# Kernel optimization log

Measured on AMD Instinct MI355X. Metric: run time of the kernel, lower is better.

The kernel has to match this reference:

```python
import jax, jax.numpy as jnp
import numpy as np

N_SEQ = 512      # n: number of generation steps (rows of x_tensor)
N_POOL = 4096    # candidate node pool size (rows of f_tensor / a_tensor)
N_FEAT = 20
E = 64           # n_node_embed
G = 128          # n_graph_embed
S = 16           # n_seq_embed
ALPHA = 20       # n_seq_alphabets


def setup_inputs() -> dict:
    key = jax.random.key(0)
    ks = jax.random.split(key, 16)
    f32 = jnp.float32

    def lin(k, fan_in, shape):
        return jax.random.normal(k, shape, f32) / jnp.sqrt(jnp.asarray(fan_in, f32))

    return {
        "x_tensor": jax.random.normal(ks[0], (N_SEQ, ALPHA), f32),
        "f_tensor": jax.random.normal(ks[1], (N_POOL, N_FEAT), f32),
        "a_tensor": jax.random.uniform(ks[2], (N_POOL, N_POOL), f32),
        "d_tensor": jax.random.uniform(ks[3], (N_POOL, N_POOL), f32),
        "w_feat": lin(ks[4], N_FEAT, (N_FEAT, E)),
        "b_feat": lin(ks[5], N_FEAT, (E,)),
        "w_gcn1": lin(ks[6], E, (E, E)),   # GCN W1, bias=False
        "w_gcn2": lin(ks[7], E, (E, E)),   # GCN W1, bias=False
        "w_graph": lin(ks[8], E, (E, G)),
        "b_graph": lin(ks[9], E, (G,)),
        "w_gate": lin(ks[10], E, (E, G)),
        "b_gate": lin(ks[11], E, (G,)),
        "w_edge": lin(ks[12], 2 * E + S + G, (2 * E + S + G, 1)),
        "b_edge": lin(ks[13], 2 * E + S + G, (1,)),
        "w_seq": lin(ks[14], ALPHA, (ALPHA, S)),
        "b_seq": lin(ks[15], ALPHA, (S,)),
    }


def reference(x_tensor, f_tensor, a_tensor, d_tensor,
              w_feat, b_feat, w_gcn1, w_gcn2,
              w_graph, b_graph, w_gate, b_gate,
              w_edge, b_edge, w_seq, b_seq):
    n = x_tensor.shape[0]
    Np = f_tensor.shape[0]
    e = w_feat.shape[1]
    g_dim = w_graph.shape[1]

    seq_embed = x_tensor @ w_seq + b_seq                 # [n, S]
    f_nodes_in = f_tensor @ w_feat + b_feat              # [Np, E]
    dAd = (d_tensor @ a_tensor) @ d_tensor               # gcn1: D A D
    h_nodes_in = (dAd @ jax.nn.relu(f_nodes_in)) @ w_gcn1  # [Np, E]

    # Chain graph at step k has k+1 nodes; A = I + sub/super diagonals.
    # Degrees: 1 (k==0), 2 at endpoints, 3 interior. Dh[k, i] = deg^{-1/2}, masked.
    ii = jnp.arange(n)
    kk = ii[:, None]
    jj = ii[None, :]
    deg = jnp.where((jj == 0) | (jj == kk), 2.0, 3.0)
    deg = jnp.where(kk == 0, 1.0, deg)
    Dh = jnp.where(jj <= kk, deg ** -0.5, 0.0).astype(x_tensor.dtype)  # [n, n]

    def step(carry, k):
        mask, idxs, h_last, h_graph = carry
        z = jnp.concatenate([
            h_nodes_in,
            jnp.broadcast_to(h_last, (Np, e)),
            jnp.broadcast_to(seq_embed[k], (Np, seq_embed.shape[1])),
            jnp.broadcast_to(h_graph, (Np, g_dim)),
        ], axis=1)                                        # [Np, 2E+S+G]
        score = ((jax.nn.relu(z) * mask[:, None]) @ w_edge)[:, 0] + b_edge[0]
        idx = jnp.argmax(score)
        mask = mask.at[idx].set(0.0)
        idxs = idxs.at[k].set(idx.astype(jnp.int32))

        # gcn2 on the chain graph over the k+1 selected nodes (band-structured).
        F_sel = f_nodes_in[idxs]                          # [n, E]; rows > k masked by dh
        dh = Dh[k]                                        # [n]
        gmat = dh[:, None] * F_sel
        g_up = jnp.pad(gmat, ((0, 1), (0, 0)))[1:]        # g[i+1]
        g_dn = jnp.pad(gmat, ((1, 0), (0, 0)))[:-1]       # g[i-1]
        dF = dh[:, None] * (gmat + g_up + g_dn)           # (D A D) F on the chain
        h_nodes = dF @ w_gcn2                             # [n, E]; rows > k are zero
        h_last_new = jnp.take(h_nodes, k, axis=0)

        valid = (jnp.arange(n) <= k).astype(h_nodes.dtype)[:, None]
        hg = h_nodes @ w_graph + b_graph
        gg = h_nodes @ w_gate + b_gate
        h_graph_new = jnp.sum(hg * jax.nn.sigmoid(gg) * valid, axis=0)
        return (mask, idxs, h_last_new, h_graph_new), score

    init = (jnp.ones(Np, x_tensor.dtype),
            jnp.zeros(n, jnp.int32),
            jnp.zeros(e, x_tensor.dtype),
            jnp.zeros(g_dim, x_tensor.dtype))
    (_, idxs, _, _), scores = jax.lax.scan(step, init, jnp.arange(n))
    return scores, idxs
```

## Files before the change

kernel.cpp:

```cpp
#include <hip/hip_runtime.h>
#include <math.h>

#define NPOOL 4096
#define NSEQ  512
#define NF    20
#define EDIM  64
#define GDIM  128
#define SDIM  16
#define ALPH  20
#define SPLITK 16
#define KSLICE (NPOOL / SPLITK)

__device__ __forceinline__ double relu_d(double x){ return x > 0.0 ? x : 0.0; }
__device__ __forceinline__ double sigm_d(double x){ return 1.0 / (1.0 + exp(-x)); }

__global__ __launch_bounds__(256) void k_prep(const float* __restrict__ f, const float* __restrict__ wf,
                       const float* __restrict__ bf, double* __restrict__ Fin, double* __restrict__ R,
                       double* __restrict__ T1z) {
    int t = blockIdx.x * 256 + threadIdx.x;
    int i = t >> 6, e = t & 63;
    double acc = (double)bf[e];
#pragma unroll
    for (int j = 0; j < NF; ++j)
        acc += (double)f[i * NF + j] * (double)wf[j * EDIM + e];
    Fin[t] = acc;
    R[t] = acc > 0.0 ? acc : 0.0;
    T1z[t] = 0.0;
}

__global__ __launch_bounds__(256) void k_seqe(const float* __restrict__ x, const float* __restrict__ wsq,
                       const float* __restrict__ bsq, double* __restrict__ seqe, int* __restrict__ rank) {
    int t = blockIdx.x * 256 + threadIdx.x;
    int k = t >> 4, s = t & 15;
    double acc = (double)bsq[s];
#pragma unroll
    for (int q = 0; q < ALPH; ++q)
        acc += (double)x[k * ALPH + q] * (double)wsq[q * SDIM + s];
    seqe[t] = acc;
    if (t < NPOOL) rank[t] = 1 << 30;
}

__global__ __launch_bounds__(256) void k_zero(double* __restrict__ buf) {
    buf[(size_t)blockIdx.x * 256 + threadIdx.x] = 0.0;
}

__global__ __launch_bounds__(256, 4) void gemm_f64_v3(const float* __restrict__ A, const double* __restrict__ B,
                                                      double* __restrict__ C) {
    __shared__ double As[32][66];
    __shared__ double Bs[32][66];
    int t  = threadIdx.x;
    int tx = t & 15;
    int ty = t >> 4;
    int row0 = blockIdx.x * 64;
    int k0   = blockIdx.y * KSLICE;
    double acc[4][4] = {};
    for (int kt = k0; kt < k0 + KSLICE; kt += 32) {
        {
            int r = t >> 2, kq = t & 3;
            const float* Ap = A + (size_t)(row0 + r) * NPOOL + kt + kq * 8;
            float4 f0 = *(const float4*)Ap;
            float4 f1 = *(const float4*)(Ap + 4);
            int kb = kq * 8;
            As[kb + 0][r] = (double)f0.x; As[kb + 1][r] = (double)f0.y;
            As[kb + 2][r] = (double)f0.z; As[kb + 3][r] = (double)f0.w;
            As[kb + 4][r] = (double)f1.x; As[kb + 5][r] = (double)f1.y;
            As[kb + 6][r] = (double)f1.z; As[kb + 7][r] = (double)f1.w;
        }
#pragma unroll
        for (int it = 0; it < 8; ++it) {
            int l = t + 256 * it;
            int kr = l >> 6, cc = l & 63;
            Bs[kr][cc] = B[(size_t)(kt + kr) * 64 + cc];
        }
        __syncthreads();
#pragma unroll
        for (int kk = 0; kk < 32; ++kk) {
            double2 a01 = *(const double2*)&As[kk][2 * ty];
            double2 a23 = *(const double2*)&As[kk][2 * ty + 32];
            double2 b01 = *(const double2*)&Bs[kk][2 * tx];
            double2 b23 = *(const double2*)&Bs[kk][2 * tx + 32];
            double a[4] = {a01.x, a01.y, a23.x, a23.y};
            double b[4] = {b01.x, b01.y, b23.x, b23.y};
#pragma unroll
            for (int i = 0; i < 4; ++i)
#pragma unroll
                for (int j = 0; j < 4; ++j)
                    acc[i][j] = fma(a[i], b[j], acc[i][j]);
        }
        __syncthreads();
    }
    int rr[4] = {2 * ty, 2 * ty + 1, 2 * ty + 32, 2 * ty + 33};
    int cc[4] = {2 * tx, 2 * tx + 1, 2 * tx + 32, 2 * tx + 33};
#pragma unroll
    for (int i = 0; i < 4; ++i)
#pragma unroll
        for (int j = 0; j < 4; ++j)
            unsafeAtomicAdd(&C[(size_t)(row0 + rr[i]) * 64 + cc[j]], acc[i][j]);
}

__global__ __launch_bounds__(256) void k_head(const double* __restrict__ T3, const float* __restrict__ w1,
                       const float* __restrict__ we, double* __restrict__ s) {
    int row = (blockIdx.x * 256 + threadIdx.x) >> 6;
    int e = threadIdx.x & 63;
    const double* r = T3 + (size_t)row * 64;
    double h = 0.0;
#pragma unroll
    for (int c = 0; c < 64; ++c)
        h += r[c] * (double)w1[c * 64 + e];
    double p = (h > 0.0 ? h : 0.0) * (double)we[e];
    for (int off = 32; off; off >>= 1) p += __shfl_down(p, off, 64);
    if (e == 0) s[row] = p;
}

__global__ __launch_bounds__(1024) void k_sort2(const double* __restrict__ s, int* __restrict__ order,
                        double* __restrict__ skey, int* __restrict__ orderB) {
    __shared__ unsigned long long keys[NPOOL];
    __shared__ int idxs[NPOOL];
    __shared__ unsigned long long ck[1024];
    __shared__ int ci[1024];
    __shared__ unsigned int hist[256];
    __shared__ unsigned int cntHi, cntEq;
    __shared__ unsigned long long prefix_s;
    __shared__ int K_s, fb_s;
    int t = threadIdx.x;
    for (int i = t; i < NPOOL; i += 1024) {
        double v = s[i] + 0.0;
        unsigned long long b = (unsigned long long)__double_as_longlong(v);
        unsigned long long m = (b >> 63) ? ~0ULL : 0x8000000000000000ULL;
        keys[i] = b ^ m;
        idxs[i] = i;
    }
    if (t == 0) { prefix_s = 0ULL; K_s = NSEQ; fb_s = 0; cntHi = 0; cntEq = 0; }
    __syncthreads();
    for (int shift = 56; shift >= 0; shift -= 8) {
        if (t < 256) hist[t] = 0;
        __syncthreads();
        unsigned long long pre = prefix_s;
        unsigned long long hmask = (shift == 56) ? 0ULL : (~0ULL << (shift + 8));
        for (int i = t; i < NPOOL; i += 1024) {
            unsigned long long kv = keys[i];
            if ((kv & hmask) == pre)
                atomicAdd(&hist[(unsigned)(kv >> shift) & 255u], 1u);
        }
        __syncthreads();
        if (t == 0) {
            int K = K_s;
            int cum = 0, b = 255;
            for (; b >= 0; --b) { cum += (int)hist[b]; if (cum >= K) break; }
            if (b < 0) { fb_s = 1; b = 0; }
            K_s = K - (cum - (int)hist[b]);
            prefix_s |= ((unsigned long long)(unsigned)b << shift);
        }
        __syncthreads();
    }
    unsigned long long T = prefix_s;
    for (int i = t; i < NPOOL; i += 1024) {
        unsigned long long kv = keys[i];
        if (kv > T) {
            unsigned p = atomicAdd(&cntHi, 1u);
            if (p < 1024u) { ck[p] = kv; ci[p] = i; }
        }
    }
    __syncthreads();
    unsigned base = cntHi;
    for (int i = t; i < NPOOL; i += 1024) {
        if (keys[i] == T) {
            unsigned p = atomicAdd(&cntEq, 1u);
            if (base + p < 1024u) { ck[base + p] = T; ci[base + p] = i; }
        }
    }
    __syncthreads();
    if (t == 0) {
        unsigned tot = cntHi + cntEq;
        if (cntHi >= (unsigned)NSEQ || tot < (unsigned)NSEQ || tot > 1024u) fb_s = 1;
    }
    __syncthreads();
    if (fb_s == 0) {
        unsigned tot = cntHi + cntEq;
        for (int i = (int)tot + t; i < 1024; i += 1024) { ck[i] = 0ULL; ci[i] = 0x7fffffff; }
        __syncthreads();
        for (int k2 = 2; k2 <= 1024; k2 <<= 1) {
            for (int j = k2 >> 1; j > 0; j >>= 1) {
                int l = t ^ j;
                if (l > t) {
                    unsigned long long ka = ck[t], kb = ck[l];
                    int ia = ci[t], ib = ci[l];
                    bool aBefore = (ka > kb) || (ka == kb && ia < ib);
                    bool asc = ((t & k2) == 0);
                    if (asc ? !aBefore : aBefore) { ck[t] = kb; ck[l] = ka; ci[t] = ib; ci[l] = ia; }
                }
                __syncthreads();
            }
        }
        if (t < NSEQ) {
            int id = ci[t];
            order[t] = id; skey[t] = s[id]; orderB[t] = ci[0];
        }
    } else {
        for (int k2 = 2; k2 <= NPOOL; k2 <<= 1) {
            for (int j = k2 >> 1; j > 0; j >>= 1) {
                for (int tt = t; tt < NPOOL; tt += 1024) {
                    int l = tt ^ j;
                    if (l > tt) {
                        unsigned long long ka = keys[tt], kb = keys[l];
                        int ia = idxs[tt], ib = idxs[l];
                        bool aBefore = (ka > kb) || (ka == kb && ia < ib);
                        bool asc = ((tt & k2) == 0);
                        if (asc ? !aBefore : aBefore) { keys[tt] = kb; keys[l] = ka; idxs[tt] = ib; idxs[l] = ia; }
                    }
                }
                __syncthreads();
            }
        }
        for (int tt = t; tt < NSEQ; tt += 1024) {
            int id = idxs[tt];
            order[tt] = id; skey[tt] = s[id]; orderB[tt] = idxs[0];
        }
    }
}

__global__ __launch_bounds__(256) void k_perk2(const double* __restrict__ Fin, const int* __restrict__ orderA,
                       const int* __restrict__ orderBv,
                       const float* __restrict__ w2, const float* __restrict__ wgr, const float* __restrict__ bgr,
                       const float* __restrict__ wga, const float* __restrict__ bga,
                       double* __restrict__ phi_inf, double* __restrict__ phi_pair, double* __restrict__ hlast) {
    const double r2 = 0.70710678118654752440;
    const double r3 = 0.57735026918962576451;
    __shared__ double u[4][64];
    __shared__ double comb[3][64];
    __shared__ double v[3][64];
    __shared__ double hgg[3][2][GDIM];
    int which = blockIdx.x >> 9;
    int k = blockIdx.x & (NSEQ - 1);
    const int* order = which ? orderBv : orderA;
    double* pi = phi_inf  + (size_t)which * NSEQ * GDIM;
    double* pp = phi_pair + (size_t)which * NSEQ * GDIM;
    double* hl = hlast    + (size_t)which * NSEQ * 64;
    int t = threadIdx.x;
    {
        int w = t >> 6, e = t & 63;
        int j = k - 3 + w;
        u[w][e] = (j >= 0) ? Fin[(size_t)order[j] * 64 + e] : 0.0;
    }
    __syncthreads();
    if (t < 192) {
        int w = t >> 6, e = t & 63;
        double dh_km3 = (k - 3 == 0) ? r2 : r3;
        double dh_km2 = (k - 2 == 0) ? r2 : r3;
        double dh_km1 = (k - 1 == 0) ? r2 : r3;
        double outer, c0, c1, c2, c3;
        if (w == 0) {
            outer = dh_km2; c0 = dh_km3; c1 = dh_km2; c2 = dh_km1; c3 = 0.0;
        } else if (w == 1) {
            outer = dh_km1; c0 = 0.0; c1 = dh_km2; c2 = dh_km1; c3 = r2;
        } else {
            if (k == 0) { outer = 1.0; c0 = c1 = c2 = 0.0; c3 = 1.0; }
            else        { outer = r2;  c0 = c1 = 0.0; c2 = dh_km1; c3 = r2; }
        }
        comb[w][e] = outer * (c0 * u[0][e] + c1 * u[1][e] + c2 * u[2][e] + c3 * u[3][e]);
    }
    __syncthreads();
    if (t < 192) {
        int w = t >> 6, e = t & 63;
        double acc = 0.0;
#pragma unroll
        for (int j = 0; j < 64; ++j)
            acc += comb[w][j] * (double)w2[j * 64 + e];
        v[w][e] = acc;
    }
    __syncthreads();
    for (int rep = 0; rep < 3; ++rep) {
        int d = t & 127, g = t >> 7;
        const float* W = g ? wga : wgr;
        const float* B = g ? bga : bgr;
        double acc = (double)B[d];
#pragma unroll
        for (int j = 0; j < 64; ++j)
            acc += v[rep][j] * (double)W[j * GDIM + d];
        hgg[rep][g][d] = acc;
    }
    __syncthreads();
    if (t < 128) {
        if (k >= 2) pi[(size_t)(k - 2) * GDIM + t] = hgg[0][0][t] * sigm_d(hgg[0][1][t]);
        double ppv = hgg[2][0][t] * sigm_d(hgg[2][1][t]);
        if (k >= 1) ppv += hgg[1][0][t] * sigm_d(hgg[1][1][t]);
        pp[(size_t)k * GDIM + t] = ppv;
    } else if (t < 192) {
        hl[(size_t)k * 64 + (t - 128)] = v[2][t - 128];
    }
}

__global__ __launch_bounds__(512) void k_scan2(const double* __restrict__ phi_inf, const double* __restrict__ phi_pair,
                       double* __restrict__ hgr) {
    __shared__ double sb[NSEQ];
    int which = blockIdx.x >> 7;
    int d = blockIdx.x & (GDIM - 1), t = threadIdx.x;
    const double* pi = phi_inf  + (size_t)which * NSEQ * GDIM;
    const double* pp = phi_pair + (size_t)which * NSEQ * GDIM;
    double* hg = hgr + (size_t)which * NSEQ * GDIM;
    sb[t] = (t >= 2) ? pi[(size_t)(t - 2) * GDIM + d] : 0.0;
    for (int off = 1; off < NSEQ; off <<= 1) {
        __syncthreads();
        double add = (t >= off) ? sb[t - off] : 0.0;
        __syncthreads();
        sb[t] += add;
    }
    __syncthreads();
    hg[(size_t)t * GDIM + d] = sb[t] + pp[(size_t)t * GDIM + d];
}

__global__ __launch_bounds__(64) void k_c2(const double* __restrict__ hlast, const double* __restrict__ hgr,
                   const double* __restrict__ seqe, const float* __restrict__ we,
                   double* __restrict__ cA, double* __restrict__ cB) {
    int which = blockIdx.x >> 9;
    int k = blockIdx.x & (NSEQ - 1), j = threadIdx.x;
    const double* hl = hlast + (size_t)which * NSEQ * 64;
    const double* hg = hgr   + (size_t)which * NSEQ * GDIM;
    double* c = which ? cB : cA;
    double ts = 0.0;
    if (k > 0) {
        ts += relu_d(hl[(size_t)(k - 1) * 64 + j]) * (double)we[64 + j];
        ts += relu_d(hg[(size_t)(k - 1) * GDIM + j]) * (double)we[144 + j];
        ts += relu_d(hg[(size_t)(k - 1) * GDIM + 64 + j]) * (double)we[208 + j];
    }
    if (j < 16) ts += relu_d(seqe[(size_t)k * SDIM + j]) * (double)we[128 + j];
    for (int off = 32; off; off >>= 1) ts += __shfl_down(ts, off, 64);
    if (j == 0) c[k] = ts;
}

__global__ __launch_bounds__(512) void k_verify2(const double* __restrict__ skey, const double* __restrict__ cA,
                         const double* __restrict__ cB, int* __restrict__ flagA, int* __restrict__ flagB) {
    __shared__ int bad;
    int t = threadIdx.x;
    if (t == 0) bad = 0;
    __syncthreads();
    if (blockIdx.x == 0) {
        if (t >= 1 && !(skey[t] + cA[t] > 0.0)) atomicOr(&bad, 1);
        __syncthreads();
        if (t == 0) flagA[0] = bad;
    } else {
        if (t >= 1 && (skey[1] + cB[t] > 0.0)) atomicOr(&bad, 1);
        __syncthreads();
        if (t == 0) flagB[0] = bad;
    }
}

__global__ __launch_bounds__(512) void k_select(const int* __restrict__ flagA, const int* __restrict__ flagB,
                        const double* __restrict__ cA, const double* __restrict__ cB,
                        const int* __restrict__ order, double* __restrict__ c,
                        int* __restrict__ idxs_sel, int* __restrict__ mode) {
    int t = threadIdx.x;
    if (flagA[0] == 0) {
        c[t] = cA[t]; idxs_sel[t] = order[t];
        if (t == 0) mode[0] = 0;
    } else if (flagB[0] == 0) {
        c[t] = cB[t]; idxs_sel[t] = order[0];
        if (t == 0) mode[0] = 1;
    } else {
        if (t == 0) mode[0] = 2;
    }
}

__global__ __launch_bounds__(256) void k_fallback(const int* __restrict__ mode,
        const double* __restrict__ Fin, const int* __restrict__ order, const double* __restrict__ skey,
        const double* __restrict__ seqe,
        const float* __restrict__ w2, const float* __restrict__ wgr, const float* __restrict__ bgr,
        const float* __restrict__ wga, const float* __restrict__ bga, const float* __restrict__ we,
        int* __restrict__ idxs_sel, double* __restrict__ c) {
    if (mode[0] != 2) return;
    const double r2 = 0.70710678118654752440;
    const double r3 = 0.57735026918962576451;
    __shared__ double u[4][64];
    __shared__ double comb[3][64];
    __shared__ double v[3][64];
    __shared__ double hgg[3][2][GDIM];
    __shared__ double Phi[GDIM], hgraph[GDIM], hlastS[64];
    __shared__ int selS, ptrS, minS_;
    int t = threadIdx.x;
    if (t < 64) { u[0][t] = u[1][t] = u[2][t] = u[3][t] = 0.0; hlastS[t] = 0.0; }
    if (t < 128) { Phi[t] = 0.0; hgraph[t] = 0.0; }
    if (t == 0) { ptrS = 0; minS_ = 0x7fffffff; }
    __syncthreads();
    for (int k = 0; k < NSEQ; ++k) {
        if (t < 64) {
            int j = t;
            double ts = relu_d(hlastS[j]) * (double)we[64 + j]
                      + relu_d(hgraph[j]) * (double)we[144 + j]
                      + relu_d(hgraph[64 + j]) * (double)we[208 + j];
            if (j < 16) ts += relu_d(seqe[(size_t)k * SDIM + j]) * (double)we[128 + j];
            for (int off = 32; off; off >>= 1) ts += __shfl_down(ts, off, 64);
            if (j == 0) {
                c[k] = ts;
                int ptr = ptrS, idx;
                if (ptr == 0) { idx = order[0]; minS_ = idx; ptrS = 1; }
                else if (skey[ptr] + ts > 0.0) {
                    idx = order[ptr];
                    if (idx < minS_) minS_ = idx;
                    ptrS = ptr + 1;
                } else idx = minS_;
                selS = idx;
                idxs_sel[k] = idx;
            }
        }
        __syncthreads();
        int idx = selS;
        if (t < 64) u[k & 3][t] = Fin[(size_t)idx * 64 + t];
        __syncthreads();
        if (t < 192) {
            int w = t >> 6, e = t & 63;
            double dh_km3 = (k - 3 == 0) ? r2 : r3;
            double dh_km2 = (k - 2 == 0) ? r2 : r3;
            double dh_km1 = (k - 1 == 0) ? r2 : r3;
            double outer, c0, c1, c2, c3;
            if (w == 0) {
                outer = dh_km2; c0 = dh_km3; c1 = dh_km2; c2 = dh_km1; c3 = 0.0;
            } else if (w == 1) {
                outer = dh_km1; c0 = 0.0; c1 = dh_km2; c2 = dh_km1; c3 = r2;
            } else {
                if (k == 0) { outer = 1.0; c0 = c1 = c2 = 0.0; c3 = 1.0; }
                else        { outer = r2;  c0 = c1 = 0.0; c2 = dh_km1; c3 = r2; }
            }
            double uu0 = u[(k - 3) & 3][e], uu1 = u[(k - 2) & 3][e], uu2 = u[(k - 1) & 3][e], uu3 = u[k & 3][e];
            comb[w][e] = outer * (c0 * uu0 + c1 * uu1 + c2 * uu2 + c3 * uu3);
        }
        __syncthreads();
        if (t < 192) {
            int w = t >> 6, e = t & 63;
            double acc = 0.0;
#pragma unroll
            for (int j = 0; j < 64; ++j)
                acc += comb[w][j] * (double)w2[j * 64 + e];
            v[w][e] = acc;
        }
        __syncthreads();
        for (int rep = 0; rep < 3; ++rep) {
            int d = t & 127, g = t >> 7;
            const float* W = g ? wga : wgr;
            const float* B = g ? bga : bgr;
            double acc = (double)B[d];
#pragma unroll
            for (int j = 0; j < 64; ++j)
                acc += v[rep][j] * (double)W[j * GDIM + d];
            hgg[rep][g][d] = acc;
        }
        __syncthreads();
        if (t < 128) {
            if (k >= 2) Phi[t] += hgg[0][0][t] * sigm_d(hgg[0][1][t]);
            double hg = Phi[t] + hgg[2][0][t] * sigm_d(hgg[2][1][t]);
            if (k >= 1) hg += hgg[1][0][t] * sigm_d(hgg[1][1][t]);
            hgraph[t] = hg;
        } else if (t < 192) {
            hlastS[t - 128] = v[2][t - 128];
        }
        __syncthreads();
    }
}

__global__ __launch_bounds__(256) void k_rank_set(const int* __restrict__ idxs_sel, int* __restrict__ rank,
                           float* __restrict__ out) {
    int t = blockIdx.x * 256 + threadIdx.x;
    if (t < NSEQ) {
        atomicMin(&rank[idxs_sel[t]], t);
        out[(size_t)NSEQ * NPOOL + t] = (float)idxs_sel[t];
    }
}

__global__ __launch_bounds__(256) void k_fill(const double* __restrict__ s, const double* __restrict__ c,
                       const int* __restrict__ rank, const float* __restrict__ be, float* __restrict__ out) {
    size_t t = (size_t)blockIdx.x * 256 + threadIdx.x;
    int k = (int)(t >> 12);
    int i = (int)(t & 4095);
    double bed = (double)be[0];
    bool masked = rank[i] < k;
    out[t] = masked ? (float)bed : (float)(s[i] + c[k] + bed);
}

extern "C" void kernel_launch(void* const* d_in, const int* in_sizes, int n_in,
                              void* d_out, int out_size, void* d_ws, size_t ws_size,
                              hipStream_t stream) {
    const float* x    = (const float*)d_in[0];
    const float* f    = (const float*)d_in[1];
    const float* amat = (const float*)d_in[2];
    const float* dmat = (const float*)d_in[3];
    const float* wf   = (const float*)d_in[4];
    const float* bf   = (const float*)d_in[5];
    const float* w1   = (const float*)d_in[6];
    const float* w2   = (const float*)d_in[7];
    const float* wgr  = (const float*)d_in[8];
    const float* bgr  = (const float*)d_in[9];
    const float* wga  = (const float*)d_in[10];
    const float* bga  = (const float*)d_in[11];
    const float* we   = (const float*)d_in[12];
    const float* be   = (const float*)d_in[13];
    const float* wsq  = (const float*)d_in[14];
    const float* bsq  = (const float*)d_in[15];
    float* out = (float*)d_out;

    char* p = (char*)d_ws;
    const size_t BIG = (size_t)NPOOL * 64 * sizeof(double);
    double* BUF0 = (double*)p; p += BIG;
    double* Fin  = (double*)p; p += BIG;
    double* BUF2 = (double*)p; p += BIG;
    double* seqe = (double*)p; p += (size_t)NSEQ * SDIM * sizeof(double);
    double* s    = (double*)p; p += (size_t)NPOOL * sizeof(double);
    double* skey = (double*)p; p += (size_t)NSEQ * sizeof(double);
    double* phi_inf  = (double*)p; p += 2 * (size_t)NSEQ * GDIM * sizeof(double);
    double* phi_pair = (double*)p; p += 2 * (size_t)NSEQ * GDIM * sizeof(double);
    double* hgr   = (double*)p; p += 2 * (size_t)NSEQ * GDIM * sizeof(double);
    double* hlast = (double*)p; p += 2 * (size_t)NSEQ * 64 * sizeof(double);
    double* cA    = (double*)p; p += (size_t)NSEQ * sizeof(double);
    double* cB    = (double*)p; p += (size_t)NSEQ * sizeof(double);
    double* c     = (double*)p; p += (size_t)NSEQ * sizeof(double);
    int* order    = (int*)p; p += 2048;
    int* orderB   = (int*)p; p += 2048;
    int* idxs_sel = (int*)p; p += 2048;
    int* rank     = (int*)p; p += (size_t)NPOOL * sizeof(int);
    int* flagA    = (int*)p; p += 256;
    int* flagB    = (int*)p; p += 256;
    int* mode     = (int*)p; p += 256;

    double* R  = BUF0;
    double* T1 = BUF2;
    double* T2 = BUF0;
    double* T3 = BUF2;

    dim3 ggrid(NPOOL / 64, SPLITK);

    k_prep<<<1024, 256, 0, stream>>>(f, wf, bf, Fin, R, T1);
    k_seqe<<<32, 256, 0, stream>>>(x, wsq, bsq, seqe, rank);

    gemm_f64_v3<<<ggrid, 256, 0, stream>>>(dmat, R, T1);
    k_zero<<<1024, 256, 0, stream>>>(T2);
    gemm_f64_v3<<<ggrid, 256, 0, stream>>>(amat, T1, T2);
    k_zero<<<1024, 256, 0, stream>>>(T3);
    gemm_f64_v3<<<ggrid, 256, 0, stream>>>(dmat, T2, T3);

    k_head<<<NPOOL / 4, 256, 0, stream>>>(T3, w1, we, s);
    k_sort2<<<1, 1024, 0, stream>>>(s, order, skey, orderB);

    k_perk2<<<2 * NSEQ, 256, 0, stream>>>(Fin, order, orderB, w2, wgr, bgr, wga, bga, phi_inf, phi_pair, hlast);
    k_scan2<<<2 * GDIM, 512, 0, stream>>>(phi_inf, phi_pair, hgr);
    k_c2<<<2 * NSEQ, 64, 0, stream>>>(hlast, hgr, seqe, we, cA, cB);
    k_verify2<<<2, 512, 0, stream>>>(skey, cA, cB, flagA, flagB);

    k_select<<<1, 512, 0, stream>>>(flagA, flagB, cA, cB, order, c, idxs_sel, mode);
    k_fallback<<<1, 256, 0, stream>>>(mode, Fin, order, skey, seqe, w2, wgr, bgr, wga, bga, we, idxs_sel, c);

    k_rank_set<<<2, 256, 0, stream>>>(idxs_sel, rank, out);
    k_fill<<<(NSEQ * NPOOL) / 256, 256, 0, stream>>>(s, c, rank, be, out);
}
```

Before: 525.7 us.

## Replace radix-select sort with register/shuffle bitonic sort on packed keys

The top-K selection kernel switches from a multi-pass radix histogram plus shared-memory bitonic sort to a full 4096-element bitonic sort. Each thread holds four packed keys (truncated score bits combined with the index) in registers, using wave shuffles for small strides and shared memory only for strides of 256 and above. A tie check falls back to the exact slow sort if truncation merges distinct scores. The head kernel also stages w1 in shared memory. This aims to cut the many barriers and atomics of the single-block sort, at the cost of more compare steps over all 4096 elements.

```diff
diff --git a/kernel.cpp b/kernel.cpp
--- a/kernel.cpp
+++ b/kernel.cpp
@@ -13,6 +13,12 @@
 
 __device__ __forceinline__ double relu_d(double x){ return x > 0.0 ? x : 0.0; }
 __device__ __forceinline__ double sigm_d(double x){ return 1.0 / (1.0 + exp(-x)); }
+
+__device__ __forceinline__ unsigned long long sortable_u64(double x) {
+    x = x + 0.0;
+    unsigned long long b = (unsigned long long)__double_as_longlong(x);
+    return b ^ ((b >> 63) ? ~0ULL : 0x8000000000000000ULL);
+}
 
 __global__ __launch_bounds__(256) void k_prep(const float* __restrict__ f, const float* __restrict__ wf,
                        const float* __restrict__ bf, double* __restrict__ Fin, double* __restrict__ R,
@@ -100,122 +106,139 @@
 
 __global__ __launch_bounds__(256) void k_head(const double* __restrict__ T3, const float* __restrict__ w1,
                        const float* __restrict__ we, double* __restrict__ s) {
-    int row = (blockIdx.x * 256 + threadIdx.x) >> 6;
-    int e = threadIdx.x & 63;
+    __shared__ float w1s[64 * 64];
+    int tt = threadIdx.x;
+    for (int i = tt; i < 64 * 64; i += 256) w1s[i] = w1[i];
+    __syncthreads();
+    int row = (blockIdx.x * 256 + tt) >> 6;
+    int e = tt & 63;
     const double* r = T3 + (size_t)row * 64;
     double h = 0.0;
 #pragma unroll
     for (int c = 0; c < 64; ++c)
-        h += r[c] * (double)w1[c * 64 + e];
+        h += r[c] * (double)w1s[c * 64 + e];
     double p = (h > 0.0 ? h : 0.0) * (double)we[e];
     for (int off = 32; off; off >>= 1) p += __shfl_down(p, off, 64);
     if (e == 0) s[row] = p;
 }
 
-__global__ __launch_bounds__(1024) void k_sort2(const double* __restrict__ s, int* __restrict__ order,
+__global__ __launch_bounds__(1024) void k_sort3(const double* __restrict__ s, int* __restrict__ order,
                         double* __restrict__ skey, int* __restrict__ orderB) {
-    __shared__ unsigned long long keys[NPOOL];
-    __shared__ int idxs[NPOOL];
-    __shared__ unsigned long long ck[1024];
-    __shared__ int ci[1024];
-    __shared__ unsigned int hist[256];
-    __shared__ unsigned int cntHi, cntEq;
-    __shared__ unsigned long long prefix_s;
-    __shared__ int K_s, fb_s;
+    __shared__ unsigned long long P[NPOOL];
+    __shared__ int idxF[NPOOL];
+    __shared__ int fbS;
     int t = threadIdx.x;
-    for (int i = t; i < NPOOL; i += 1024) {
-        double v = s[i] + 0.0;
-        unsigned long long b = (unsigned long long)__double_as_longlong(v);
-        unsigned long long m = (b >> 63) ? ~0ULL : 0x8000000000000000ULL;
-        keys[i] = b ^ m;
-        idxs[i] = i;
-    }
-    if (t == 0) { prefix_s = 0ULL; K_s = NSEQ; fb_s = 0; cntHi = 0; cntEq = 0; }
-    __syncthreads();
-    for (int shift = 56; shift >= 0; shift -= 8) {
-        if (t < 256) hist[t] = 0;
-        __syncthreads();
-        unsigned long long pre = prefix_s;
-        unsigned long long hmask = (shift == 56) ? 0ULL : (~0ULL << (shift + 8));
-        for (int i = t; i < NPOOL; i += 1024) {
-            unsigned long long kv = keys[i];
-            if ((kv & hmask) == pre)
-                atomicAdd(&hist[(unsigned)(kv >> shift) & 255u], 1u);
-        }
-        __syncthreads();
-        if (t == 0) {
-            int K = K_s;
-            int cum = 0, b = 255;
-            for (; b >= 0; --b) { cum += (int)hist[b]; if (cum >= K) break; }
-            if (b < 0) { fb_s = 1; b = 0; }
-            K_s = K - (cum - (int)hist[b]);
-            prefix_s |= ((unsigned long long)(unsigned)b << shift);
-        }
-        __syncthreads();
-    }
-    unsigned long long T = prefix_s;
-    for (int i = t; i < NPOOL; i += 1024) {
-        unsigned long long kv = keys[i];
-        if (kv > T) {
-            unsigned p = atomicAdd(&cntHi, 1u);
-            if (p < 1024u) { ck[p] = kv; ci[p] = i; }
-        }
-    }
-    __syncthreads();
-    unsigned base = cntHi;
-    for (int i = t; i < NPOOL; i += 1024) {
-        if (keys[i] == T) {
-            unsigned p = atomicAdd(&cntEq, 1u);
-            if (base + p < 1024u) { ck[base + p] = T; ci[base + p] = i; }
-        }
-    }
-    __syncthreads();
-    if (t == 0) {
-        unsigned tot = cntHi + cntEq;
-        if (cntHi >= (unsigned)NSEQ || tot < (unsigned)NSEQ || tot > 1024u) fb_s = 1;
-    }
-    __syncthreads();
-    if (fb_s == 0) {
-        unsigned tot = cntHi + cntEq;
-        for (int i = (int)tot + t; i < 1024; i += 1024) { ck[i] = 0ULL; ci[i] = 0x7fffffff; }
-        __syncthreads();
-        for (int k2 = 2; k2 <= 1024; k2 <<= 1) {
-            for (int j = k2 >> 1; j > 0; j >>= 1) {
-                int l = t ^ j;
-                if (l > t) {
-                    unsigned long long ka = ck[t], kb = ck[l];
-                    int ia = ci[t], ib = ci[l];
+    if (t == 0) fbS = 0;
+    unsigned long long v[4];
+#pragma unroll
+    for (int i = 0; i < 4; ++i) {
+        int e = 4 * t + i;
+        unsigned long long srt = sortable_u64(s[e]);
+        v[i] = ((~(srt >> 12)) << 12) | (unsigned long long)e;
+    }
+
+#define SHFL_ROUND(jj, kk)                                                        \
+    {                                                                             \
+        int lm = (int)((jj) >> 2);                                                \
+        _Pragma("unroll")                                                         \
+        for (int i = 0; i < 4; ++i) {                                             \
+            unsigned long long p = (unsigned long long)__shfl_xor((long long)v[i], lm, 64); \
+            unsigned e = 4u * (unsigned)t + (unsigned)i;                          \
+            bool takeMin = (((e & (jj)) == 0u) == ((e & (kk)) == 0u));            \
+            unsigned long long mn = v[i] < p ? v[i] : p;                          \
+            unsigned long long mx = v[i] < p ? p : v[i];                          \
+            v[i] = takeMin ? mn : mx;                                             \
+        }                                                                         \
+    }
+
+#define LOCAL_ROUNDS(kk)                                                          \
+    {                                                                             \
+        if ((kk) >= 4) {                                                          \
+            _Pragma("unroll")                                                     \
+            for (int i = 0; i < 2; ++i) {                                         \
+                unsigned e = 4u * (unsigned)t + (unsigned)i;                      \
+                bool asc = ((e & (kk)) == 0u);                                    \
+                unsigned long long a = v[i], b = v[i + 2];                        \
+                bool sw = asc ? (a > b) : (a < b);                                \
+                v[i] = sw ? b : a; v[i + 2] = sw ? a : b;                         \
+            }                                                                     \
+        }                                                                         \
+        _Pragma("unroll")                                                         \
+        for (int i = 0; i < 4; i += 2) {                                          \
+            unsigned e = 4u * (unsigned)t + (unsigned)i;                          \
+            bool asc = ((e & (kk)) == 0u);                                        \
+            unsigned long long a = v[i], b = v[i + 1];                            \
+            bool sw = asc ? (a > b) : (a < b);                                    \
+            v[i] = sw ? b : a; v[i + 1] = sw ? a : b;                             \
+        }                                                                         \
+    }
+
+    for (unsigned k = 2; k <= 256; k <<= 1) {
+        for (unsigned j = k >> 1; j >= 4; j >>= 1) SHFL_ROUND(j, k)
+        LOCAL_ROUNDS(k)
+    }
+    for (unsigned k = 512; k <= 4096; k <<= 1) {
+        for (unsigned j = k >> 1; j >= 256; j >>= 1) {
+            __syncthreads();
+            P[4 * t + 0] = v[0]; P[4 * t + 1] = v[1];
+            P[4 * t + 2] = v[2]; P[4 * t + 3] = v[3];
+            __syncthreads();
+            unsigned base = (4u * (unsigned)t) ^ j;
+#pragma unroll
+            for (int i = 0; i < 4; ++i) {
+                unsigned e = 4u * (unsigned)t + (unsigned)i;
+                unsigned long long p = P[base + i];
+                bool takeMin = (((e & j) == 0u) == ((e & k) == 0u));
+                unsigned long long mn = v[i] < p ? v[i] : p;
+                unsigned long long mx = v[i] < p ? p : v[i];
+                v[i] = takeMin ? mn : mx;
+            }
+        }
+        for (unsigned j = 128; j >= 4; j >>= 1) SHFL_ROUND(j, k)
+        LOCAL_ROUNDS(k)
+    }
+#undef SHFL_ROUND
+#undef LOCAL_ROUNDS
+
+    __syncthreads();
+    P[4 * t + 0] = v[0]; P[4 * t + 1] = v[1];
+    P[4 * t + 2] = v[2]; P[4 * t + 3] = v[3];
+    __syncthreads();
+    if (t < 512) {
+        unsigned long long pa = P[t], pb = P[t + 1];
+        if ((pa >> 12) == (pb >> 12)) {
+            int ia = (int)(pa & 4095ULL), ib = (int)(pb & 4095ULL);
+            if (sortable_u64(s[ia]) != sortable_u64(s[ib])) atomicOr(&fbS, 1);
+        }
+    }
+    __syncthreads();
+    if (fbS == 0) {
+        if (t < NSEQ) {
+            int id = (int)(P[t] & 4095ULL);
+            order[t] = id; skey[t] = s[id]; orderB[t] = (int)(P[0] & 4095ULL);
+        }
+        return;
+    }
+    for (int i = t; i < NPOOL; i += 1024) { P[i] = sortable_u64(s[i]); idxF[i] = i; }
+    __syncthreads();
+    for (int k2 = 2; k2 <= NPOOL; k2 <<= 1) {
+        for (int j = k2 >> 1; j > 0; j >>= 1) {
+            for (int tt = t; tt < NPOOL; tt += 1024) {
+                int l = tt ^ j;
+                if (l > tt) {
+                    unsigned long long ka = P[tt], kb = P[l];
+                    int ia = idxF[tt], ib = idxF[l];
                     bool aBefore = (ka > kb) || (ka == kb && ia < ib);
-                    bool asc = ((t & k2) == 0);
-                    if (asc ? !aBefore : aBefore) { ck[t] = kb; ck[l] = ka; ci[t] = ib; ci[l] = ia; }
+                    bool asc = ((tt & k2) == 0);
+                    if (asc ? !aBefore : aBefore) { P[tt] = kb; P[l] = ka; idxF[tt] = ib; idxF[l] = ia; }
                 }
-                __syncthreads();
             }
-        }
-        if (t < NSEQ) {
-            int id = ci[t];
-            order[t] = id; skey[t] = s[id]; orderB[t] = ci[0];
-        }
-    } else {
-        for (int k2 = 2; k2 <= NPOOL; k2 <<= 1) {
-            for (int j = k2 >> 1; j > 0; j >>= 1) {
-                for (int tt = t; tt < NPOOL; tt += 1024) {
-                    int l = tt ^ j;
-                    if (l > tt) {
-                        unsigned long long ka = keys[tt], kb = keys[l];
-                        int ia = idxs[tt], ib = idxs[l];
-                        bool aBefore = (ka > kb) || (ka == kb && ia < ib);
-                        bool asc = ((tt & k2) == 0);
-                        if (asc ? !aBefore : aBefore) { keys[tt] = kb; keys[l] = ka; idxs[tt] = ib; idxs[l] = ia; }
-                    }
-                }
-                __syncthreads();
-            }
-        }
-        for (int tt = t; tt < NSEQ; tt += 1024) {
-            int id = idxs[tt];
-            order[tt] = id; skey[tt] = s[id]; orderB[tt] = idxs[0];
-        }
+            __syncthreads();
+        }
+    }
+    for (int tt = t; tt < NSEQ; tt += 1024) {
+        int id = idxF[tt];
+        order[tt] = id; skey[tt] = s[id]; orderB[tt] = idxF[0];
     }
 }
 
@@ -536,7 +559,7 @@
     gemm_f64_v3<<<ggrid, 256, 0, stream>>>(dmat, T2, T3);
 
     k_head<<<NPOOL / 4, 256, 0, stream>>>(T3, w1, we, s);
-    k_sort2<<<1, 1024, 0, stream>>>(s, order, skey, orderB);
+    k_sort3<<<1, 1024, 0, stream>>>(s, order, skey, orderB);
 
     k_perk2<<<2 * NSEQ, 256, 0, stream>>>(Fin, order, orderB, w2, wgr, bgr, wga, bga, phi_inf, phi_pair, hlast);
     k_scan2<<<2 * GDIM, 512, 0, stream>>>(phi_inf, phi_pair, hgr);
```

Measured after the change: 467.3 us. 11.1% less time.
